# Kernel tuning notes

Hardware: AMD Instinct MI355X
Metric: run time of the kernel (lower is better)

The kernel has to match this reference:

```python
import jax, jax.numpy as jnp
import numpy as np

D = 2048
H = 16
DH = D // H  # 128
THETA = 10000.0

def _rope(x, pos):
    # x: (..., S, DH); pos: (S,) absolute positions
    freqs = 1.0 / THETA ** (jnp.arange(0, DH, 2, dtype=jnp.float32) / DH)  # (DH/2,)
    emb = pos[:, None].astype(jnp.float32) * freqs[None, :]                # (S, DH/2)
    cos = jnp.concatenate([jnp.cos(emb), jnp.cos(emb)], axis=-1)          # tile like torch .repeat(...,2)
    sin = jnp.concatenate([jnp.sin(emb), jnp.sin(emb)], axis=-1)
    x1, x2 = x[..., : DH // 2], x[..., DH // 2 :]
    rot = jnp.concatenate([-x2, x1], axis=-1)  # rotate_half
    return x * cos + rot * sin

def setup_inputs() -> dict:
    key = jax.random.key(0)
    ks = jax.random.split(key, 4)
    B, S = 2, 2048
    return {
        "x": jax.random.normal(ks[0], (B, S, D), jnp.float32),
        "wq": 0.01 * jax.random.normal(ks[1], (D, D), jnp.float32),
        "wkv": 0.01 * jax.random.normal(ks[2], (D, 2 * DH), jnp.float32),
        "wo": 0.01 * jax.random.normal(ks[3], (D, D), jnp.float32),
        "past_length": 0,
    }

def reference(x, wq, wkv, wo, past_length):
    B, S, _ = x.shape
    Q = x @ wq.T                       # (B,S,D)
    KV = x @ wkv                       # (B,S,2*DH)
    K, V = KV[..., :DH], KV[..., DH:]  # single shared KV head (B,S,DH)
    # no kv_cache (prefill): S_full = past_length + S with past_length=0
    S_full = past_length + S
    q = Q.reshape(B, S, H, DH).transpose(0, 2, 1, 3)   # (B,H,S,DH)
    q = _rope(q, past_length + jnp.arange(S))
    k = _rope(K, jnp.arange(S_full))                    # (B,S_full,DH), unreplicated
    scores = jnp.einsum('bhsd,btd->bhst', q, k) / np.float32(np.sqrt(DH))
    i = jnp.arange(S)[:, None]
    j = jnp.arange(S_full)[None, :]
    causal = j <= i + past_length                       # tril(diagonal=past_length)
    scores = jnp.where(causal[None, None], scores, -jnp.inf)
    attn = jax.nn.softmax(scores, axis=-1)
    o = jnp.einsum('bhst,btd->bhsd', attn, V)           # (B,H,S,DH)
    o = o.transpose(0, 2, 1, 3).reshape(B, S, D)
    out = o @ wo.T
    return (out, K, V)  # output + updated kv cache
```

## Files before the change

### kernel.cpp

```cpp
#include <hip/hip_runtime.h>
#include <hip/hip_bf16.h>
#include <cstdint>


typedef __attribute__((ext_vector_type(8))) __bf16 bf16x8;
typedef __attribute__((ext_vector_type(4))) float f32x4;
typedef __attribute__((ext_vector_type(16))) float f32x16;
typedef __attribute__((ext_vector_type(4))) float floatv4;
typedef __attribute__((ext_vector_type(4))) unsigned short ushortv4;
typedef __attribute__((ext_vector_type(4))) unsigned int uintv4;

__device__ __forceinline__ unsigned short f2bf(float f) {
    union { float f; unsigned u; } v; v.f = f;
    unsigned r = v.u + 0x7fffu + ((v.u >> 16) & 1u);
    return (unsigned short)(r >> 16);
}

__device__ __forceinline__ unsigned pk2(float a, float b) {
    return (unsigned)f2bf(a) | ((unsigned)f2bf(b) << 16);
}

__device__ __forceinline__ f32x16 zero16() {
    f32x16 z;
#pragma unroll
    for (int i = 0; i < 16; ++i) z[i] = 0.f;
    return z;
}

#define GLL16(g, l)                                                                   \
    __builtin_amdgcn_global_load_lds(                                                 \
        (const __attribute__((address_space(1))) void*)(uintptr_t)(g),                \
        (__attribute__((address_space(3))) void*)(unsigned)(uintptr_t)(l), 16, 0, 0)

__global__ __launch_bounds__(256) void cast_bf16_k(const float* __restrict__ src,
                                                   unsigned short* __restrict__ dst, int n4) {
    int i = blockIdx.x * 256 + threadIdx.x;
    if (i >= n4) return;
    floatv4 v = reinterpret_cast<const floatv4*>(src)[i];
    ushortv4 o;
    o.x = f2bf(v.x); o.y = f2bf(v.y); o.z = f2bf(v.z); o.w = f2bf(v.w);
    reinterpret_cast<ushortv4*>(dst)[i] = o;
}

__global__ __launch_bounds__(256) void cast_t_wkv_k(const float* __restrict__ src,
                                                    unsigned short* __restrict__ dst) {
    int i = blockIdx.x * 256 + threadIdx.x;
    int k = i >> 8, j = i & 255;
    dst[j * 2048 + k] = f2bf(src[i]);
}

__global__ __launch_bounds__(256) void gemm_bt(const unsigned short* __restrict__ A,
                                               const unsigned short* __restrict__ B,
                                               float* __restrict__ C,
                                               int M, int N, int K) {
    __shared__ __align__(16) unsigned short As[4096];
    __shared__ __align__(16) unsigned short Bs[4096];
    const int tid  = threadIdx.x;
    const int lane = tid & 63;
    const int wid  = tid >> 6;
    const int wr   = wid >> 1;
    const int wc   = wid & 1;
    const size_t row0 = (size_t)blockIdx.y * 128;
    const size_t col0 = (size_t)blockIdx.x * 128;
    f32x4 acc[4][4];
#pragma unroll
    for (int m = 0; m < 4; ++m)
#pragma unroll
        for (int n = 0; n < 4; ++n) acc[m][n] = (f32x4){0.f, 0.f, 0.f, 0.f};

    const int srow = tid >> 2;
    const int scol = (tid & 3) << 3;
    const unsigned short* Ag = A + (row0 + srow) * (size_t)K + scol;
    const unsigned short* Bg = B + (col0 + srow) * (size_t)K + scol;
    unsigned short* AsW = &As[wid << 9];
    unsigned short* BsW = &Bs[wid << 9];

    const int lrow = lane & 15;
    const int lk   = (lane >> 4) << 3;

    for (int k0 = 0; k0 < K; k0 += 32) {
        GLL16(Ag + k0, AsW);
        GLL16(Ag + k0 + (size_t)64 * K, AsW + 2048);
        GLL16(Bg + k0, BsW);
        GLL16(Bg + k0 + (size_t)64 * K, BsW + 2048);
        __syncthreads();
        bf16x8 af[4], bfr[4];
#pragma unroll
        for (int m = 0; m < 4; ++m)
            af[m] = *reinterpret_cast<const bf16x8*>(&As[(wr * 64 + m * 16 + lrow) * 32 + lk]);
#pragma unroll
        for (int n = 0; n < 4; ++n)
            bfr[n] = *reinterpret_cast<const bf16x8*>(&Bs[(wc * 64 + n * 16 + lrow) * 32 + lk]);
#pragma unroll
        for (int m = 0; m < 4; ++m)
#pragma unroll
            for (int n = 0; n < 4; ++n)
                acc[m][n] = __builtin_amdgcn_mfma_f32_16x16x32_bf16(af[m], bfr[n], acc[m][n], 0, 0, 0);
        __syncthreads();
    }
    const size_t orow0 = row0 + wr * 64 + ((lane >> 4) << 2);
    const size_t ocol  = col0 + wc * 64 + lrow;
#pragma unroll
    for (int m = 0; m < 4; ++m)
#pragma unroll
        for (int n = 0; n < 4; ++n)
#pragma unroll
            for (int r = 0; r < 4; ++r)
                C[(orow0 + m * 16 + r) * (size_t)N + ocol + n * 16] = acc[m][n][r];
}

__global__ __launch_bounds__(256) void rope_pack_k(const float* __restrict__ Qf,
                                                   const float* __restrict__ KVf,
                                                   unsigned short* __restrict__ Qb,
                                                   unsigned short* __restrict__ Kb,
                                                   unsigned short* __restrict__ Vt,
                                                   float* __restrict__ Kout,
                                                   float* __restrict__ Vout) {
    const int row = blockIdx.x;
    const int b = row >> 11;
    const int s = row & 2047;
    const int t = threadIdx.x;
    const float* qrow = Qf + (size_t)row * 2048;
#pragma unroll
    for (int it = 0; it < 4; ++it) {
        int p = t + it * 256;
        int h = p >> 6;
        int i = p & 63;
        float fr  = exp2f(-(float)i * 0.20762050593045858f);
        float ang = (float)s * fr;
        float sn, c;
        sincosf(ang, &sn, &c);
        float x1 = qrow[h * 128 + i];
        float x2 = qrow[h * 128 + i + 64];
        size_t qb = (((size_t)(b * 16 + h)) * 2048 + s) * 128;
        Qb[qb + i]      = f2bf(x1 * c - x2 * sn);
        Qb[qb + i + 64] = f2bf(x2 * c + x1 * sn);
    }
    const float* kvrow = KVf + (size_t)row * 256;
    if (t < 128) {
        float kv = kvrow[t];
        float vv = kvrow[128 + t];
        Kout[(size_t)row * 128 + t] = kv;
        Vout[(size_t)row * 128 + t] = vv;
        Vt[((size_t)(b * 128 + t)) * 2048 + s] = f2bf(vv);
    }
    if (t < 64) {
        float fr  = exp2f(-(float)t * 0.20762050593045858f);
        float ang = (float)s * fr;
        float sn, c;
        sincosf(ang, &sn, &c);
        float x1 = kvrow[t];
        float x2 = kvrow[t + 64];
        size_t ko = ((size_t)b * 2048 + s) * 128;
        Kb[ko + t]      = f2bf(x1 * c - x2 * sn);
        Kb[ko + t + 64] = f2bf(x2 * c + x1 * sn);
    }
}

__global__ __launch_bounds__(256, 2) void attn_k(const unsigned short* __restrict__ Qb,
                                                 const unsigned short* __restrict__ Kb,
                                                 const unsigned short* __restrict__ Vt,
                                                 unsigned short* __restrict__ Ob) {
    const int h = blockIdx.y, b = blockIdx.z;
    const int lane = threadIdx.x & 63;
    const int w = threadIdx.x >> 6;
    const int tb = blockIdx.x * 4 + w;
    const int t = b ? (63 - tb) : tb;
    const int q0 = t * 32;
    const int lq = lane & 31;
    const int hl = lane >> 5;
    const int kofs = hl * 8;

    const unsigned short* qp = Qb + (((size_t)(b * 16 + h)) * 2048 + q0 + lq) * 128 + kofs;
    bf16x8 qf[8];
#pragma unroll
    for (int c = 0; c < 8; ++c)
        qf[c] = *reinterpret_cast<const bf16x8*>(qp + 16 * c);

    f32x16 O[4];
#pragma unroll
    for (int dt = 0; dt < 4; ++dt) O[dt] = zero16();
    float m = -1e30f, l = 0.f;

    const int nkt = t / 2 + 1;
    const unsigned short* kb = Kb + (size_t)b * 2048 * 128;
    const unsigned short* vb = Vt + (size_t)b * 128 * 2048;
    const float csc = 0.12751782377892224f;

    bf16x8 bufA[16], bufB[16];
    {
        const unsigned short* kp = kb + (size_t)lq * 128 + kofs;
#pragma unroll
        for (int c = 0; c < 8; ++c) {
            bufA[c]     = *reinterpret_cast<const bf16x8*>(kp + 16 * c);
            bufA[8 + c] = *reinterpret_cast<const bf16x8*>(kp + 32 * 128 + 16 * c);
        }
    }

    int kt = 0;
    auto STEP = [&](bf16x8 (&Kc)[16], bf16x8 (&Kn)[16]) {
        f32x16 S0 = zero16(), S1 = zero16();
#pragma unroll
        for (int c = 0; c < 8; ++c) {
            S0 = __builtin_amdgcn_mfma_f32_32x32x16_bf16(Kc[c],     qf[c], S0, 0, 0, 0);
            S1 = __builtin_amdgcn_mfma_f32_32x32x16_bf16(Kc[8 + c], qf[c], S1, 0, 0, 0);
        }
        const unsigned short* vp = vb + (size_t)lq * 2048 + 64 * kt + kofs;
#pragma unroll
        for (int dt = 0; dt < 4; ++dt)
#pragma unroll
            for (int kc = 0; kc < 4; ++kc)
                Kc[4 * dt + kc] =
                    *reinterpret_cast<const bf16x8*>(vp + (size_t)(32 * dt) * 2048 + 16 * kc);
        const int ktn = (kt + 1 < nkt) ? (kt + 1) : kt;
        const unsigned short* kp = kb + (size_t)(64 * ktn + lq) * 128 + kofs;
#pragma unroll
        for (int c = 0; c < 8; ++c) {
            Kn[c]     = *reinterpret_cast<const bf16x8*>(kp + 16 * c);
            Kn[8 + c] = *reinterpret_cast<const bf16x8*>(kp + 32 * 128 + 16 * c);
        }
        float sc[32];
        const bool lastt = (kt == nkt - 1);
#pragma unroll
        for (int s = 0; s < 2; ++s)
#pragma unroll
            for (int r = 0; r < 16; ++r) {
                float v = (s ? S1[r] : S0[r]) * csc;
                if (lastt) {
                    int key = 64 * kt + 32 * s + (r & 3) + 8 * (r >> 2) + 4 * hl;
                    if (key > q0 + lq) v = -3.0e38f;
                }
                sc[16 * s + r] = v;
            }
        float tm[16];
#pragma unroll
        for (int i = 0; i < 16; ++i) tm[i] = fmaxf(sc[i], sc[i + 16]);
#pragma unroll
        for (int st = 8; st > 0; st >>= 1)
#pragma unroll
            for (int i = 0; i < st; ++i) tm[i] = fmaxf(tm[i], tm[i + st]);
        float mt = fmaxf(tm[0], __shfl_xor(tm[0], 32));
        float mn = fmaxf(m, mt);
        float corr = __builtin_amdgcn_exp2f(m - mn);
        m = mn;
#pragma unroll
        for (int i = 0; i < 32; ++i) sc[i] = __builtin_amdgcn_exp2f(sc[i] - mn);
        float ts[16];
#pragma unroll
        for (int i = 0; i < 16; ++i) ts[i] = sc[i] + sc[i + 16];
#pragma unroll
        for (int st = 8; st > 0; st >>= 1)
#pragma unroll
            for (int i = 0; i < st; ++i) ts[i] += ts[i + st];
        l = l * corr + ts[0] + __shfl_xor(ts[0], 32);
#pragma unroll
        for (int dt = 0; dt < 4; ++dt)
#pragma unroll
            for (int r = 0; r < 16; ++r) O[dt][r] *= corr;
        unsigned pw[4][4];
#pragma unroll
        for (int s = 0; s < 2; ++s)
#pragma unroll
            for (int c2 = 0; c2 < 2; ++c2) {
                const int rb = 16 * s + 8 * c2;
                unsigned X0 = pk2(sc[rb + 0], sc[rb + 1]);
                unsigned X1 = pk2(sc[rb + 2], sc[rb + 3]);
                unsigned X2 = pk2(sc[rb + 4], sc[rb + 5]);
                unsigned X3 = pk2(sc[rb + 6], sc[rb + 7]);
                unsigned y0 = __shfl_xor(X0, 32);
                unsigned y1 = __shfl_xor(X1, 32);
                unsigned y2 = __shfl_xor(X2, 32);
                unsigned y3 = __shfl_xor(X3, 32);
                const int kc = 2 * s + c2;
                pw[kc][0] = hl ? y2 : X0;
                pw[kc][1] = hl ? y3 : X1;
                pw[kc][2] = hl ? X2 : y0;
                pw[kc][3] = hl ? X3 : y1;
            }
#pragma unroll
        for (int kc = 0; kc < 4; ++kc) {
            uintv4 u;
            u.x = pw[kc][0]; u.y = pw[kc][1]; u.z = pw[kc][2]; u.w = pw[kc][3];
            bf16x8 pf = __builtin_bit_cast(bf16x8, u);
#pragma unroll
            for (int dt = 0; dt < 4; ++dt)
                O[dt] = __builtin_amdgcn_mfma_f32_32x32x16_bf16(Kc[4 * dt + kc], pf, O[dt], 0, 0, 0);
        }
    };

    for (;;) {
        STEP(bufA, bufB);
        if (++kt == nkt) break;
        STEP(bufB, bufA);
        if (++kt == nkt) break;
    }

    float invl = 1.f / l;
    unsigned short* ob = Ob + ((size_t)(b * 2048 + q0 + lq)) * 2048 + h * 128;
#pragma unroll
    for (int dt = 0; dt < 4; ++dt)
#pragma unroll
        for (int g = 0; g < 4; ++g) {
            ushortv4 ov;
            ov.x = f2bf(O[dt][4 * g + 0] * invl);
            ov.y = f2bf(O[dt][4 * g + 1] * invl);
            ov.z = f2bf(O[dt][4 * g + 2] * invl);
            ov.w = f2bf(O[dt][4 * g + 3] * invl);
            *reinterpret_cast<ushortv4*>(ob + 32 * dt + 8 * g + 4 * hl) = ov;
        }
}

extern "C" void kernel_launch(void* const* d_in, const int* in_sizes, int n_in,
                              void* d_out, int out_size, void* d_ws, size_t ws_size,
                              hipStream_t stream) {
    const float* x   = (const float*)d_in[0];
    const float* wq  = (const float*)d_in[1];
    const float* wkv = (const float*)d_in[2];
    const float* wo  = (const float*)d_in[3];

    float* out  = (float*)d_out;
    float* Kout = out + 8388608;
    float* Vout = Kout + 524288;

    char* ws = (char*)d_ws;
    unsigned short* xb   = (unsigned short*)(ws + 0);
    unsigned short* wqb  = (unsigned short*)(ws + 16777216);
    unsigned short* wkvT = (unsigned short*)(ws + 25165824);
    unsigned short* wob  = (unsigned short*)(ws + 26214400);
    float*          KVf  = (float*)(ws + 34603008);
    float*          Qf   = (float*)(ws + 38797312);
    unsigned short* Qb   = (unsigned short*)(ws + 0);
    unsigned short* Kb   = (unsigned short*)(ws + 16777216);
    unsigned short* Vt   = (unsigned short*)(ws + 17825792);
    unsigned short* Ob   = (unsigned short*)(ws + 34603008);

    cast_bf16_k<<<8192, 256, 0, stream>>>(x,  xb,  2097152);
    cast_bf16_k<<<4096, 256, 0, stream>>>(wq, wqb, 1048576);
    cast_bf16_k<<<4096, 256, 0, stream>>>(wo, wob, 1048576);
    cast_t_wkv_k<<<2048, 256, 0, stream>>>(wkv, wkvT);

    gemm_bt<<<dim3(2, 32),  256, 0, stream>>>(xb, wkvT, KVf, 4096, 256,  2048);
    gemm_bt<<<dim3(16, 32), 256, 0, stream>>>(xb, wqb,  Qf,  4096, 2048, 2048);

    rope_pack_k<<<4096, 256, 0, stream>>>(Qf, KVf, Qb, Kb, Vt, Kout, Vout);

    attn_k<<<dim3(16, 16, 2), 256, 0, stream>>>(Qb, Kb, Vt, Ob);

    gemm_bt<<<dim3(16, 32), 256, 0, stream>>>(Ob, wob, out, 4096, 2048, 2048);
}
```

Baseline: 433.5 us.

## Split attention KV range across wave pairs and merge partial softmax via LDS

Each block now holds two query tiles, one light and one heavy under the causal mask, so per-block work is balanced. Each tile is processed by two waves that split its key tiles in half. The first wave writes its partial O, m and l to shared memory, and the second merges them with rescaled exponentials before writing the output. The grid doubles, which raises parallelism and shortens the critical path per tile. The cost is extra LDS traffic, a block-wide barrier and 32KB of shared memory, which may reduce occupancy.

```diff
diff --git a/kernel.cpp b/kernel.cpp
--- a/kernel.cpp
+++ b/kernel.cpp
@@ -164,13 +164,18 @@
     const int h = blockIdx.y, b = blockIdx.z;
     const int lane = threadIdx.x & 63;
     const int w = threadIdx.x >> 6;
-    const int tb = blockIdx.x * 4 + w;
-    const int t = b ? (63 - tb) : tb;
+    const int pair = w >> 1;
+    const int role = w & 1;
+    const int t = pair ? (63 - blockIdx.x) : blockIdx.x;
     const int q0 = t * 32;
     const int lq = lane & 31;
     const int hl = lane >> 5;
     const int kofs = hl * 8;
 
+    __shared__ float Olds[2][4][16][64];
+    __shared__ float mlds[2][32];
+    __shared__ float llds[2][32];
+
     const unsigned short* qp = Qb + (((size_t)(b * 16 + h)) * 2048 + q0 + lq) * 128 + kofs;
     bf16x8 qf[8];
 #pragma unroll
@@ -183,13 +188,16 @@
     float m = -1e30f, l = 0.f;
 
     const int nkt = t / 2 + 1;
+    const int nh  = (nkt + 1) / 2;
+    const int ks  = role ? nh : 0;
+    const int ke  = role ? nkt : nh;
     const unsigned short* kb = Kb + (size_t)b * 2048 * 128;
     const unsigned short* vb = Vt + (size_t)b * 128 * 2048;
     const float csc = 0.12751782377892224f;
 
     bf16x8 bufA[16], bufB[16];
-    {
-        const unsigned short* kp = kb + (size_t)lq * 128 + kofs;
+    if (ks < ke) {
+        const unsigned short* kp = kb + (size_t)(64 * ks + lq) * 128 + kofs;
 #pragma unroll
         for (int c = 0; c < 8; ++c) {
             bufA[c]     = *reinterpret_cast<const bf16x8*>(kp + 16 * c);
@@ -197,7 +205,7 @@
         }
     }
 
-    int kt = 0;
+    int kt = ks;
     auto STEP = [&](bf16x8 (&Kc)[16], bf16x8 (&Kn)[16]) {
         f32x16 S0 = zero16(), S1 = zero16();
 #pragma unroll
@@ -212,7 +220,7 @@
             for (int kc = 0; kc < 4; ++kc)
                 Kc[4 * dt + kc] =
                     *reinterpret_cast<const bf16x8*>(vp + (size_t)(32 * dt) * 2048 + 16 * kc);
-        const int ktn = (kt + 1 < nkt) ? (kt + 1) : kt;
+        const int ktn = (kt + 1 < ke) ? (kt + 1) : kt;
         const unsigned short* kp = kb + (size_t)(64 * ktn + lq) * 128 + kofs;
 #pragma unroll
         for (int c = 0; c < 8; ++c) {
@@ -288,26 +296,44 @@
         }
     };
 
-    for (;;) {
+    while (kt < ke) {
         STEP(bufA, bufB);
-        if (++kt == nkt) break;
+        if (++kt == ke) break;
         STEP(bufB, bufA);
-        if (++kt == nkt) break;
-    }
-
-    float invl = 1.f / l;
-    unsigned short* ob = Ob + ((size_t)(b * 2048 + q0 + lq)) * 2048 + h * 128;
-#pragma unroll
-    for (int dt = 0; dt < 4; ++dt)
-#pragma unroll
-        for (int g = 0; g < 4; ++g) {
-            ushortv4 ov;
-            ov.x = f2bf(O[dt][4 * g + 0] * invl);
-            ov.y = f2bf(O[dt][4 * g + 1] * invl);
-            ov.z = f2bf(O[dt][4 * g + 2] * invl);
-            ov.w = f2bf(O[dt][4 * g + 3] * invl);
-            *reinterpret_cast<ushortv4*>(ob + 32 * dt + 8 * g + 4 * hl) = ov;
-        }
+        ++kt;
+    }
+
+    if (role == 0) {
+#pragma unroll
+        for (int dt = 0; dt < 4; ++dt)
+#pragma unroll
+            for (int r = 0; r < 16; ++r)
+                Olds[pair][dt][r][lane] = O[dt][r];
+        if (lane < 32) { mlds[pair][lane] = m; llds[pair][lane] = l; }
+    }
+    __syncthreads();
+    if (role == 1) {
+        float mA = mlds[pair][lq];
+        float lA = llds[pair][lq];
+        float ms = fmaxf(mA, m);
+        float sA = __builtin_amdgcn_exp2f(mA - ms);
+        float sB = __builtin_amdgcn_exp2f(m - ms);
+        float invl = 1.f / (lA * sA + l * sB);
+        unsigned short* ob = Ob + ((size_t)(b * 2048 + q0 + lq)) * 2048 + h * 128;
+#pragma unroll
+        for (int dt = 0; dt < 4; ++dt)
+#pragma unroll
+            for (int g = 0; g < 4; ++g) {
+                ushortv4 ov;
+#pragma unroll
+                for (int j = 0; j < 4; ++j) {
+                    int r = 4 * g + j;
+                    float val = (Olds[pair][dt][r][lane] * sA + O[dt][r] * sB) * invl;
+                    ((unsigned short*)&ov)[j] = f2bf(val);
+                }
+                *reinterpret_cast<ushortv4*>(ob + 32 * dt + 8 * g + 4 * hl) = ov;
+            }
+    }
 }
 
 extern "C" void kernel_launch(void* const* d_in, const int* in_sizes, int n_in,
@@ -344,7 +370,7 @@
 
     rope_pack_k<<<4096, 256, 0, stream>>>(Qf, KVf, Qb, Kb, Vt, Kout, Vout);
 
-    attn_k<<<dim3(16, 16, 2), 256, 0, stream>>>(Qb, Kb, Vt, Ob);
+    attn_k<<<dim3(32, 16, 2), 256, 0, stream>>>(Qb, Kb, Vt, Ob);
 
     gemm_bt<<<dim3(16, 32), 256, 0, stream>>>(Ob, wob, out, 4096, 2048, 2048);
 }
```

Result: faster. 416.6 us (-3.9%).
